# Kernel tuning notes

Hardware: AMD Instinct MI355X
Metric: run time of the kernel (lower is better)

The kernel has to match this reference:

```python
import jax, jax.numpy as jnp
import numpy as np

ALPHA = 0.2  # LeakyReLU negative slope


def setup_inputs() -> dict:
    key = jax.random.key(0)
    k1, k2, k3, k4 = jax.random.split(key, 4)
    bs, n, fin = 8, 1024, 256
    heads, fo = 8, 64
    h = jax.random.normal(k1, (bs, n, fin), dtype=jnp.float32)
    adj = jax.random.randint(k2, (bs, n, n), 0, 2, dtype=jnp.int32)
    # W stored as [in_features, heads*out] so Wh = h @ W (same math as torch Linear)
    W = jax.random.normal(k3, (fin, heads * fo), dtype=jnp.float32) * 0.1
    a = jax.random.normal(k4, (heads, 2 * fo), dtype=jnp.float32) * 0.1
    return {"h": h, "adj": adj, "W": W, "a": a}


def reference(h, adj, W, a):
    bs, n, _ = h.shape
    heads, two_fo = a.shape
    fo = two_fo // 2
    # Wh: [bs, n, heads, fo]
    Wh = (h @ W).reshape(bs, n, heads, fo)
    a_src, a_dst = a[:, :fo], a[:, fo:]
    # Additive attention decomposed: e[b,h,i,j] = leaky_relu(src[b,h,i] + dst[b,h,j])
    e_src = jnp.einsum('bnhf,hf->bhn', Wh, a_src)  # [bs, heads, n]
    e_dst = jnp.einsum('bnhf,hf->bhn', Wh, a_dst)
    e = e_src[:, :, :, None] + e_dst[:, :, None, :]  # [bs, heads, n, n]
    e = jnp.where(e > 0, e, ALPHA * e)  # LeakyReLU
    e = jnp.where(adj[:, None, :, :] == 0, -jnp.inf, e)
    attn = jax.nn.softmax(e, axis=-1)  # [bs, heads, n, n]
    # h_prime[b,i,h,f] = sum_j attn[b,h,i,j] * Wh[b,j,h,f]
    h_prime = jnp.einsum('bhij,bjhf->bihf', attn, Wh)
    return h_prime.reshape(bs, n, heads * fo)
```

## Files before the change

kernel.cpp:

```cpp
#include <hip/hip_runtime.h>
#include <hip/hip_bf16.h>
#include <math.h>

#define BS 8
#define NN 1024
#define FIN 256
#define HEADS 8
#define FO 64
#define NH (HEADS*FO)
static constexpr float ALPHA = 0.2f;
static constexpr float LOG2E = 1.4426950408889634f;

typedef short bf16x8 __attribute__((ext_vector_type(8)));
typedef float f32x4  __attribute__((ext_vector_type(4)));
typedef unsigned short u16;
typedef unsigned u32;
typedef u16 u16x4v __attribute__((ext_vector_type(4)));
typedef u16 u16x8v __attribute__((ext_vector_type(8)));

__device__ __forceinline__ u16 f2b(float x) {
    __hip_bfloat16 b = __float2bfloat16(x);
    return *reinterpret_cast<u16*>(&b);
}
__device__ __forceinline__ float fexp2(float x) {
#if __has_builtin(__builtin_amdgcn_exp2f)
    return __builtin_amdgcn_exp2f(x);
#else
    float r; asm("v_exp_f32 %0, %1" : "=v"(r) : "v"(x)); return r;
#endif
}
__device__ __forceinline__ void gload_lds16(const void* g, void* l) {
    __builtin_amdgcn_global_load_lds(
        (const __attribute__((address_space(1))) unsigned int*)g,
        (__attribute__((address_space(3))) unsigned int*)l, 16, 0, 0);
}

__global__ __launch_bounds__(256) void prep_misc(const float* __restrict__ h,
                                                 const int* __restrict__ adj,
                                                 const float* __restrict__ W,
                                                 u16* __restrict__ hb,
                                                 u16* __restrict__ WbT,
                                                 u32* __restrict__ bits) {
    const int bid = blockIdx.x;
    const int t = threadIdx.x;
    if (bid < 8192) {
        const int lane = t & 63;
        const size_t e0 = ((size_t)bid * 256 + t) * 4;
        const int4 v = *reinterpret_cast<const int4*>(adj + e0);
        u32 x = (v.x ? 1u : 0u) | (v.y ? 2u : 0u) | (v.z ? 4u : 0u) | (v.w ? 8u : 0u);
        {   const u32 r = (u32)__shfl_xor((int)x, 1);
            const int sh = (lane & 1) * 4;  x = (x << sh) | (r << (4 - sh)); }
        {   const u32 r = (u32)__shfl_xor((int)x, 2);
            const int sh = (lane & 2) * 4;  x = (x << sh) | (r << (8 - sh)); }
        {   const u32 r = (u32)__shfl_xor((int)x, 4);
            const int sh = (lane & 4) * 4;  x = (x << sh) | (r << (16 - sh)); }
        if ((lane & 7) == 0) bits[e0 >> 5] = x;
    } else if (bid < 9216) {
        const int i = ((bid - 8192) * 256 + t) * 8;
        const float4 v0 = *reinterpret_cast<const float4*>(h + i);
        const float4 v1 = *reinterpret_cast<const float4*>(h + i + 4);
        u16x8v o;
        o[0]=f2b(v0.x); o[1]=f2b(v0.y); o[2]=f2b(v0.z); o[3]=f2b(v0.w);
        o[4]=f2b(v1.x); o[5]=f2b(v1.y); o[6]=f2b(v1.z); o[7]=f2b(v1.w);
        *reinterpret_cast<u16x8v*>(hb + i) = o;
    } else {
        __shared__ float T[64][65];
        const int bb = bid - 9216;
        const int hh = bb & 7;
        const int n0 = hh * 64, k0 = (bb >> 3) * 64;
        const int r4 = t >> 6, c = t & 63;
        #pragma unroll
        for (int p = 0; p < 16; ++p) {
            const int r = p * 4 + r4;
            T[r][c] = W[(size_t)(k0 + r) * NH + n0 + c];
        }
        __syncthreads();
        #pragma unroll
        for (int p = 0; p < 16; ++p) {
            const int r = p * 4 + r4;
            WbT[(size_t)(n0 + r) * FIN + k0 + c] = f2b(T[c][r]);
        }
    }
}

__global__ __launch_bounds__(256) void gemm_whT(const u16* __restrict__ hb,
                                                const u16* __restrict__ WbT,
                                                const float* __restrict__ avec,
                                                u16* __restrict__ WhT,
                                                float* __restrict__ esrc,
                                                float* __restrict__ edst) {
    __shared__ u16 Al[2][64 * 64];
    __shared__ u16 Bl[2][64 * 64];
    const int t = threadIdx.x, wv = t >> 6, lane = t & 63;
    const int g = lane >> 4, l15 = lane & 15;
    const int lid = (blockIdx.x & 7) * 128 + (blockIdx.x >> 3);
    const int m0 = (lid >> 3) * 64;
    const int h  = lid & 7;
    const int lr = lane >> 3;
    const int sch = (lane & 7) ^ lr;
    const int bh = (m0 >> 10) * HEADS + h;

    f32x4 acc[4] = {};

    auto stageA = [&](int buf, int k0) {
        #pragma unroll
        for (int c = 0; c < 2; ++c) {
            const int rowb = wv * 16 + c * 8;
            gload_lds16(hb + (size_t)(m0 + rowb + lr) * FIN + k0 + sch * 8,
                        &Al[buf][rowb * 64]);
        }
    };
    auto stageB = [&](int buf, int k0) {
        #pragma unroll
        for (int c = 0; c < 2; ++c) {
            const int rowb = wv * 16 + c * 8;
            gload_lds16(WbT + (size_t)(h * 64 + rowb + lr) * FIN + k0 + sch * 8,
                        &Bl[buf][rowb * 64]);
        }
    };

    stageA(0, 0); stageB(0, 0);
    __syncthreads();
    for (int kt = 0; kt < 4; ++kt) {
        const int buf = kt & 1;
        if (kt < 3) { stageA(buf ^ 1, (kt + 1) * 64); stageB(buf ^ 1, (kt + 1) * 64); }
        #pragma unroll
        for (int ks = 0; ks < 2; ++ks) {
            const int ch = (ks * 4 + g) ^ (l15 & 7);
            const bf16x8 afr = *reinterpret_cast<const bf16x8*>(
                &Al[buf][(wv * 16 + l15) * 64 + ch * 8]);
            #pragma unroll
            for (int n = 0; n < 4; ++n) {
                const bf16x8 bfr = *reinterpret_cast<const bf16x8*>(
                    &Bl[buf][(n * 16 + l15) * 64 + ch * 8]);
                acc[n] = __builtin_amdgcn_mfma_f32_16x16x32_bf16(afr, bfr, acc[n], 0, 0, 0);
            }
        }
        __syncthreads();
    }

    {
        float as_[4], ad_[4];
        #pragma unroll
        for (int n = 0; n < 4; ++n) {
            as_[n] = avec[h * 128 + n * 16 + l15] * LOG2E;
            ad_[n] = avec[h * 128 + 64 + n * 16 + l15] * LOG2E;
        }
        #pragma unroll
        for (int r = 0; r < 4; ++r) {
            float ps = acc[0][r] * as_[0] + acc[1][r] * as_[1]
                     + acc[2][r] * as_[2] + acc[3][r] * as_[3];
            float pd = acc[0][r] * ad_[0] + acc[1][r] * ad_[1]
                     + acc[2][r] * ad_[2] + acc[3][r] * ad_[3];
            #pragma unroll
            for (int off = 1; off < 16; off <<= 1) {
                ps += __shfl_xor(ps, off);
                pd += __shfl_xor(pd, off);
            }
            if (l15 == 0) {
                const int i = (m0 + wv * 16 + g * 4 + r) & (NN - 1);
                esrc[(size_t)bh * NN + i] = ps;
                edst[(size_t)bh * NN + i] = pd;
            }
        }
    }

    u16* scr = &Al[0][0];
    #pragma unroll
    for (int n = 0; n < 4; ++n) {
        u16x4v pk;
        #pragma unroll
        for (int r = 0; r < 4; ++r) pk[r] = f2b(acc[n][r]);
        *reinterpret_cast<u16x4v*>(&scr[(n * 16 + l15) * 72 + wv * 16 + g * 4]) = pk;
    }
    __syncthreads();
    const int il0 = m0 & (NN - 1);
    const int f = t >> 2, q = t & 3;
    const u16x8v v0 = *reinterpret_cast<const u16x8v*>(&scr[f * 72 + q * 16]);
    const u16x8v v1 = *reinterpret_cast<const u16x8v*>(&scr[f * 72 + q * 16 + 8]);
    u16* dst = &WhT[((size_t)bh * 64 + f) * NN + il0 + q * 16];
    *reinterpret_cast<u16x8v*>(dst)     = v0;
    *reinterpret_cast<u16x8v*>(dst + 8) = v1;
}

__global__ __launch_bounds__(128, 4) void attn_pv(const u32* __restrict__ bits,
                                                  const u16* __restrict__ WhT,
                                                  const float* __restrict__ esrc,
                                                  const float* __restrict__ edst,
                                                  float* __restrict__ out) {
    __shared__ u16 Bs[2][64 * 64];
    const int t = threadIdx.x, wv = t >> 6, lane = t & 63;
    const int g = lane >> 4, l15 = lane & 15;
    const int lr = lane >> 3, sch = (lane & 7) ^ lr;

    const int lid = (blockIdx.x & 7) * 256 + (blockIdx.x >> 3);
    const int it = lid & 31, h = (lid >> 5) & 7, b = lid >> 8;
    const int i0 = it * 32;
    const int bh = b * HEADS + h;
    const int rowi = i0 + wv * 16 + l15;

    const float es = esrc[(size_t)bh * NN + rowi];
    const u16*  whb = WhT + (size_t)bh * 64 * NN;
    const float* ed = edst + (size_t)bh * NN + 8 * g;
    const u32*  bitrow = bits + (size_t)(b * NN + rowi) * 32;

    auto stageB = [&](int buf, int j0) {
        #pragma unroll
        for (int c = 0; c < 4; ++c) {
            const int fb = wv * 32 + c * 8;
            gload_lds16(whb + (size_t)(fb + lr) * NN + j0 + sch * 8,
                        &Bs[buf][fb * 64]);
        }
    };

    stageB(0, 0);
    float4 peA[2], peB[2];
    u32    pwS[2];
    #pragma unroll
    for (int s = 0; s < 2; ++s) {
        peA[s] = *(const float4*)(ed + s * 32);
        peB[s] = *(const float4*)(ed + s * 32 + 4);
        pwS[s] = bitrow[s];
    }
    __syncthreads();

    f32x4 acc[4] = {};
    f32x4 dsum = {};
    bf16x8 ones;
    #pragma unroll
    for (int q = 0; q < 8; ++q) ones[q] = (short)0x3F80;

    for (int tt = 0; tt < 16; ++tt) {
        const int buf = tt & 1;
        const bool more = (tt < 15);
        if (more) {
            stageB(buf ^ 1, (tt + 1) * 64);
            asm volatile("" ::: "memory");
        }
        #pragma unroll
        for (int ks = 0; ks < 2; ++ks) {
            const int s = tt * 2 + ks;
            const float4 e0 = peA[ks], e1 = peB[ks];
            const u32 word = pwS[ks];
            if (more) {
                peA[ks] = *(const float4*)(ed + (s + 2) * 32);
                peB[ks] = *(const float4*)(ed + (s + 2) * 32 + 4);
                pwS[ks] = bitrow[s + 2];
            }
            const int chb = ((ks * 4 + g) ^ (l15 & 7)) * 8;
            const bf16x8 v0 = *(const bf16x8*)(&Bs[buf][(0 * 16 + l15) * 64 + chb]);
            const bf16x8 v1 = *(const bf16x8*)(&Bs[buf][(1 * 16 + l15) * 64 + chb]);
            const bf16x8 v2 = *(const bf16x8*)(&Bs[buf][(2 * 16 + l15) * 64 + chb]);
            const bf16x8 v3 = *(const bf16x8*)(&Bs[buf][(3 * 16 + l15) * 64 + chb]);

            const u32 byte_ = (word >> (8 * g)) & 0xffu;
            float ps[8];
            {
                float sv;
                sv = es + e0.x; sv = fmaxf(sv, ALPHA * sv); sv = (byte_ & 1u)        ? sv : -1e30f; ps[0] = fexp2(sv);
                sv = es + e0.y; sv = fmaxf(sv, ALPHA * sv); sv = ((byte_ >> 1) & 1u) ? sv : -1e30f; ps[1] = fexp2(sv);
                sv = es + e0.z; sv = fmaxf(sv, ALPHA * sv); sv = ((byte_ >> 2) & 1u) ? sv : -1e30f; ps[2] = fexp2(sv);
                sv = es + e0.w; sv = fmaxf(sv, ALPHA * sv); sv = ((byte_ >> 3) & 1u) ? sv : -1e30f; ps[3] = fexp2(sv);
                sv = es + e1.x; sv = fmaxf(sv, ALPHA * sv); sv = ((byte_ >> 4) & 1u) ? sv : -1e30f; ps[4] = fexp2(sv);
                sv = es + e1.y; sv = fmaxf(sv, ALPHA * sv); sv = ((byte_ >> 5) & 1u) ? sv : -1e30f; ps[5] = fexp2(sv);
                sv = es + e1.z; sv = fmaxf(sv, ALPHA * sv); sv = ((byte_ >> 6) & 1u) ? sv : -1e30f; ps[6] = fexp2(sv);
                sv = es + e1.w; sv = fmaxf(sv, ALPHA * sv); sv = ((byte_ >> 7) & 1u) ? sv : -1e30f; ps[7] = fexp2(sv);
            }
            union { u32 u[4]; bf16x8 v; } af;
            #pragma unroll
            for (int qp = 0; qp < 4; ++qp) {
                union { __hip_bfloat162 b2; u32 w; } cv;
                cv.b2 = __float22bfloat162_rn(make_float2(ps[2*qp], ps[2*qp+1]));
                af.u[qp] = cv.w;
            }
            __builtin_amdgcn_s_setprio(1);
            acc[0] = __builtin_amdgcn_mfma_f32_16x16x32_bf16(af.v, v0, acc[0], 0, 0, 0);
            acc[1] = __builtin_amdgcn_mfma_f32_16x16x32_bf16(af.v, v1, acc[1], 0, 0, 0);
            acc[2] = __builtin_amdgcn_mfma_f32_16x16x32_bf16(af.v, v2, acc[2], 0, 0, 0);
            acc[3] = __builtin_amdgcn_mfma_f32_16x16x32_bf16(af.v, v3, acc[3], 0, 0, 0);
            dsum   = __builtin_amdgcn_mfma_f32_16x16x32_bf16(af.v, ones, dsum, 0, 0, 0);
            __builtin_amdgcn_s_setprio(0);
        }
        if (more) {
            asm volatile("s_waitcnt vmcnt(6)" ::: "memory");
            __builtin_amdgcn_s_barrier();
        }
    }

    float inv[4];
    #pragma unroll
    for (int r = 0; r < 4; ++r) inv[r] = 1.0f / dsum[r];
    #pragma unroll
    for (int n = 0; n < 4; ++n)
        #pragma unroll
        for (int r = 0; r < 4; ++r) {
            const int io = i0 + wv * 16 + g * 4 + r;
            out[(size_t)(b * NN + io) * NH + h * 64 + n * 16 + l15] =
                acc[n][r] * inv[r];
        }
}

extern "C" void kernel_launch(void* const* d_in, const int* in_sizes, int n_in,
                              void* d_out, int out_size, void* d_ws, size_t ws_size,
                              hipStream_t stream) {
    const float* h   = (const float*)d_in[0];
    const int*   adj = (const int*)  d_in[1];
    const float* W   = (const float*)d_in[2];
    const float* a   = (const float*)d_in[3];
    float* out = (float*)d_out;

    char* p = (char*)d_ws;
    u16*   hb   = (u16*)p;   p += (size_t)BS * NN * FIN * 2;
    u16*   WbT  = (u16*)p;   p += (size_t)NH * FIN * 2;
    u16*   WhT  = (u16*)p;   p += (size_t)BS * HEADS * FO * NN * 2;
    float* esrc = (float*)p; p += (size_t)BS * HEADS * NN * 4;
    float* edst = (float*)p; p += (size_t)BS * HEADS * NN * 4;
    u32*   bits = (u32*)p;

    prep_misc<<<9248, 256, 0, stream>>>(h, adj, W, hb, WbT, bits);
    gemm_whT <<<1024, 256, 0, stream>>>(hb, WbT, a, WhT, esrc, edst);
    attn_pv  <<<2048, 128, 0, stream>>>(bits, WhT, esrc, edst, out);
}
```

Before: 51.35 us.

## Enlarge attention tile to 128 rows per block with two row-groups per wave

The attention-PV kernel now runs 4 waves per block, each handling 32 query rows instead of 16, so a block covers 128 rows. Each staged WhT tile in shared memory and each LDS B-fragment read is reused across two MFMA row groups. This cuts the global and LDS traffic per output row and the number of blocks. In exchange the kernel uses more registers per wave (two accumulator sets), has fewer blocks (512) to spread across CUs, and its wait count was adjusted to match the new load count.

```diff
diff --git a/kernel.cpp b/kernel.cpp
--- a/kernel.cpp
+++ b/kernel.cpp
@@ -183,7 +183,7 @@
     *reinterpret_cast<u16x8v*>(dst + 8) = v1;
 }
 
-__global__ __launch_bounds__(128, 4) void attn_pv(const u32* __restrict__ bits,
+__global__ __launch_bounds__(256, 2) void attn_pv(const u32* __restrict__ bits,
                                                   const u16* __restrict__ WhT,
                                                   const float* __restrict__ esrc,
                                                   const float* __restrict__ edst,
@@ -193,21 +193,23 @@
     const int g = lane >> 4, l15 = lane & 15;
     const int lr = lane >> 3, sch = (lane & 7) ^ lr;
 
-    const int lid = (blockIdx.x & 7) * 256 + (blockIdx.x >> 3);
-    const int it = lid & 31, h = (lid >> 5) & 7, b = lid >> 8;
-    const int i0 = it * 32;
+    const int lid = (blockIdx.x & 7) * 64 + (blockIdx.x >> 3);
+    const int it = lid & 7, h = (lid >> 3) & 7, b = lid >> 6;
+    const int i0 = it * 128;
     const int bh = b * HEADS + h;
-    const int rowi = i0 + wv * 16 + l15;
-
-    const float es = esrc[(size_t)bh * NN + rowi];
+    const int row0 = i0 + wv * 32 + l15;
+
+    const float es0 = esrc[(size_t)bh * NN + row0];
+    const float es1 = esrc[(size_t)bh * NN + row0 + 16];
     const u16*  whb = WhT + (size_t)bh * 64 * NN;
     const float* ed = edst + (size_t)bh * NN + 8 * g;
-    const u32*  bitrow = bits + (size_t)(b * NN + rowi) * 32;
+    const u32*  bitrow0 = bits + (size_t)(b * NN + row0) * 32;
+    const u32*  bitrow1 = bitrow0 + 16 * 32;
 
     auto stageB = [&](int buf, int j0) {
         #pragma unroll
-        for (int c = 0; c < 4; ++c) {
-            const int fb = wv * 32 + c * 8;
+        for (int c = 0; c < 2; ++c) {
+            const int fb = wv * 16 + c * 8;
             gload_lds16(whb + (size_t)(fb + lr) * NN + j0 + sch * 8,
                         &Bs[buf][fb * 64]);
         }
@@ -215,17 +217,18 @@
 
     stageB(0, 0);
     float4 peA[2], peB[2];
-    u32    pwS[2];
+    u32    pw0[2], pw1[2];
     #pragma unroll
     for (int s = 0; s < 2; ++s) {
         peA[s] = *(const float4*)(ed + s * 32);
         peB[s] = *(const float4*)(ed + s * 32 + 4);
-        pwS[s] = bitrow[s];
+        pw0[s] = bitrow0[s];
+        pw1[s] = bitrow1[s];
     }
     __syncthreads();
 
-    f32x4 acc[4] = {};
-    f32x4 dsum = {};
+    f32x4 acc0[4] = {}, acc1[4] = {};
+    f32x4 dsum0 = {}, dsum1 = {};
     bf16x8 ones;
     #pragma unroll
     for (int q = 0; q < 8; ++q) ones[q] = (short)0x3F80;
@@ -241,11 +244,12 @@
         for (int ks = 0; ks < 2; ++ks) {
             const int s = tt * 2 + ks;
             const float4 e0 = peA[ks], e1 = peB[ks];
-            const u32 word = pwS[ks];
+            const u32 w0 = pw0[ks], w1 = pw1[ks];
             if (more) {
                 peA[ks] = *(const float4*)(ed + (s + 2) * 32);
                 peB[ks] = *(const float4*)(ed + (s + 2) * 32 + 4);
-                pwS[ks] = bitrow[s + 2];
+                pw0[ks] = bitrow0[s + 2];
+                pw1[ks] = bitrow1[s + 2];
             }
             const int chb = ((ks * 4 + g) ^ (l15 & 7)) * 8;
             const bf16x8 v0 = *(const bf16x8*)(&Bs[buf][(0 * 16 + l15) * 64 + chb]);
@@ -253,50 +257,63 @@
             const bf16x8 v2 = *(const bf16x8*)(&Bs[buf][(2 * 16 + l15) * 64 + chb]);
             const bf16x8 v3 = *(const bf16x8*)(&Bs[buf][(3 * 16 + l15) * 64 + chb]);
 
-            const u32 byte_ = (word >> (8 * g)) & 0xffu;
-            float ps[8];
-            {
-                float sv;
-                sv = es + e0.x; sv = fmaxf(sv, ALPHA * sv); sv = (byte_ & 1u)        ? sv : -1e30f; ps[0] = fexp2(sv);
-                sv = es + e0.y; sv = fmaxf(sv, ALPHA * sv); sv = ((byte_ >> 1) & 1u) ? sv : -1e30f; ps[1] = fexp2(sv);
-                sv = es + e0.z; sv = fmaxf(sv, ALPHA * sv); sv = ((byte_ >> 2) & 1u) ? sv : -1e30f; ps[2] = fexp2(sv);
-                sv = es + e0.w; sv = fmaxf(sv, ALPHA * sv); sv = ((byte_ >> 3) & 1u) ? sv : -1e30f; ps[3] = fexp2(sv);
-                sv = es + e1.x; sv = fmaxf(sv, ALPHA * sv); sv = ((byte_ >> 4) & 1u) ? sv : -1e30f; ps[4] = fexp2(sv);
-                sv = es + e1.y; sv = fmaxf(sv, ALPHA * sv); sv = ((byte_ >> 5) & 1u) ? sv : -1e30f; ps[5] = fexp2(sv);
-                sv = es + e1.z; sv = fmaxf(sv, ALPHA * sv); sv = ((byte_ >> 6) & 1u) ? sv : -1e30f; ps[6] = fexp2(sv);
-                sv = es + e1.w; sv = fmaxf(sv, ALPHA * sv); sv = ((byte_ >> 7) & 1u) ? sv : -1e30f; ps[7] = fexp2(sv);
-            }
-            union { u32 u[4]; bf16x8 v; } af;
+            float ej[8];
+            ej[0]=e0.x; ej[1]=e0.y; ej[2]=e0.z; ej[3]=e0.w;
+            ej[4]=e1.x; ej[5]=e1.y; ej[6]=e1.z; ej[7]=e1.w;
+            const u32 by0 = (w0 >> (8 * g)) & 0xffu;
+            const u32 by1 = (w1 >> (8 * g)) & 0xffu;
+            float p0[8], p1[8];
+            #pragma unroll
+            for (int q = 0; q < 8; ++q) {
+                float s0 = es0 + ej[q];
+                float s1 = es1 + ej[q];
+                s0 = fmaxf(s0, ALPHA * s0);
+                s1 = fmaxf(s1, ALPHA * s1);
+                s0 = ((by0 >> q) & 1u) ? s0 : -1e30f;
+                s1 = ((by1 >> q) & 1u) ? s1 : -1e30f;
+                p0[q] = fexp2(s0);
+                p1[q] = fexp2(s1);
+            }
+            union { u32 u[4]; bf16x8 v; } af0, af1;
             #pragma unroll
             for (int qp = 0; qp < 4; ++qp) {
-                union { __hip_bfloat162 b2; u32 w; } cv;
-                cv.b2 = __float22bfloat162_rn(make_float2(ps[2*qp], ps[2*qp+1]));
-                af.u[qp] = cv.w;
+                union { __hip_bfloat162 b2; u32 w; } c0, c1;
+                c0.b2 = __float22bfloat162_rn(make_float2(p0[2*qp], p0[2*qp+1]));
+                c1.b2 = __float22bfloat162_rn(make_float2(p1[2*qp], p1[2*qp+1]));
+                af0.u[qp] = c0.w;
+                af1.u[qp] = c1.w;
             }
             __builtin_amdgcn_s_setprio(1);
-            acc[0] = __builtin_amdgcn_mfma_f32_16x16x32_bf16(af.v, v0, acc[0], 0, 0, 0);
-            acc[1] = __builtin_amdgcn_mfma_f32_16x16x32_bf16(af.v, v1, acc[1], 0, 0, 0);
-            acc[2] = __builtin_amdgcn_mfma_f32_16x16x32_bf16(af.v, v2, acc[2], 0, 0, 0);
-            acc[3] = __builtin_amdgcn_mfma_f32_16x16x32_bf16(af.v, v3, acc[3], 0, 0, 0);
-            dsum   = __builtin_amdgcn_mfma_f32_16x16x32_bf16(af.v, ones, dsum, 0, 0, 0);
+            acc0[0] = __builtin_amdgcn_mfma_f32_16x16x32_bf16(af0.v, v0, acc0[0], 0, 0, 0);
+            acc1[0] = __builtin_amdgcn_mfma_f32_16x16x32_bf16(af1.v, v0, acc1[0], 0, 0, 0);
+            acc0[1] = __builtin_amdgcn_mfma_f32_16x16x32_bf16(af0.v, v1, acc0[1], 0, 0, 0);
+            acc1[1] = __builtin_amdgcn_mfma_f32_16x16x32_bf16(af1.v, v1, acc1[1], 0, 0, 0);
+            acc0[2] = __builtin_amdgcn_mfma_f32_16x16x32_bf16(af0.v, v2, acc0[2], 0, 0, 0);
+            acc1[2] = __builtin_amdgcn_mfma_f32_16x16x32_bf16(af1.v, v2, acc1[2], 0, 0, 0);
+            acc0[3] = __builtin_amdgcn_mfma_f32_16x16x32_bf16(af0.v, v3, acc0[3], 0, 0, 0);
+            acc1[3] = __builtin_amdgcn_mfma_f32_16x16x32_bf16(af1.v, v3, acc1[3], 0, 0, 0);
+            dsum0   = __builtin_amdgcn_mfma_f32_16x16x32_bf16(af0.v, ones, dsum0, 0, 0, 0);
+            dsum1   = __builtin_amdgcn_mfma_f32_16x16x32_bf16(af1.v, ones, dsum1, 0, 0, 0);
             __builtin_amdgcn_s_setprio(0);
         }
         if (more) {
-            asm volatile("s_waitcnt vmcnt(6)" ::: "memory");
+            asm volatile("s_waitcnt vmcnt(8)" ::: "memory");
             __builtin_amdgcn_s_barrier();
         }
     }
 
-    float inv[4];
-    #pragma unroll
-    for (int r = 0; r < 4; ++r) inv[r] = 1.0f / dsum[r];
+    float inv0[4], inv1[4];
+    #pragma unroll
+    for (int r = 0; r < 4; ++r) { inv0[r] = 1.0f / dsum0[r]; inv1[r] = 1.0f / dsum1[r]; }
     #pragma unroll
     for (int n = 0; n < 4; ++n)
         #pragma unroll
         for (int r = 0; r < 4; ++r) {
-            const int io = i0 + wv * 16 + g * 4 + r;
-            out[(size_t)(b * NN + io) * NH + h * 64 + n * 16 + l15] =
-                acc[n][r] * inv[r];
+            const int io0 = i0 + wv * 32 + g * 4 + r;
+            out[(size_t)(b * NN + io0) * NH + h * 64 + n * 16 + l15] =
+                acc0[n][r] * inv0[r];
+            out[(size_t)(b * NN + io0 + 16) * NH + h * 64 + n * 16 + l15] =
+                acc1[n][r] * inv1[r];
         }
 }
 
@@ -319,5 +336,5 @@
 
     prep_misc<<<9248, 256, 0, stream>>>(h, adj, W, hb, WbT, bits);
     gemm_whT <<<1024, 256, 0, stream>>>(hb, WbT, a, WhT, esrc, edst);
-    attn_pv  <<<2048, 128, 0, stream>>>(bits, WhT, esrc, edst, out);
-}
+    attn_pv  <<<512, 256, 0, stream>>>(bits, WhT, esrc, edst, out);
+}
```

Result: faster. 50.30 us (-2.0%).

## Remap attn_pv so each wave owns a head with private V buffers, no barriers

Applied to the files above, without the earlier changes.

The attention-PV kernel now gives each 256-thread block 16 query rows and 4 heads, with one wave per head. Each wave streams its own V tiles into a private double-buffered LDS region, so the per-iteration block barrier is dropped. The adjacency bit words for the 16 rows are loaded into shared memory once and shared across the four head-waves, rather than fetched per wave from global memory. The trade-offs are a smaller 16-row tile per wave, 32 narrower pipeline steps, and reliance on the vmcnt wait alone to keep the intra-wave LDS double buffering correct.

```diff
diff --git a/kernel.cpp b/kernel.cpp
--- a/kernel.cpp
+++ b/kernel.cpp
@@ -183,46 +183,57 @@
     *reinterpret_cast<u16x8v*>(dst + 8) = v1;
 }
 
-__global__ __launch_bounds__(128, 4) void attn_pv(const u32* __restrict__ bits,
+__global__ __launch_bounds__(256, 4) void attn_pv(const u32* __restrict__ bits,
                                                   const u16* __restrict__ WhT,
                                                   const float* __restrict__ esrc,
                                                   const float* __restrict__ edst,
                                                   float* __restrict__ out) {
-    __shared__ u16 Bs[2][64 * 64];
+    __shared__ u16 Vb[4][2][2048];
+    __shared__ u32 bitsT[32][16];
+
     const int t = threadIdx.x, wv = t >> 6, lane = t & 63;
     const int g = lane >> 4, l15 = lane & 15;
-    const int lr = lane >> 3, sch = (lane & 7) ^ lr;
-
-    const int lid = (blockIdx.x & 7) * 256 + (blockIdx.x >> 3);
-    const int it = lid & 31, h = (lid >> 5) & 7, b = lid >> 8;
-    const int i0 = it * 32;
+
+    const int lid = (blockIdx.x & 7) * 128 + (blockIdx.x >> 3);
+    const int it = lid & 63;
+    const int combo = lid >> 6;
+    const int b = combo >> 1, hg = combo & 1;
+    const int i0 = it * 16;
+    const int h  = hg * 4 + wv;
     const int bh = b * HEADS + h;
-    const int rowi = i0 + wv * 16 + l15;
-
-    const float es = esrc[(size_t)bh * NN + rowi];
+
+    const float es = esrc[(size_t)bh * NN + i0 + l15];
     const u16*  whb = WhT + (size_t)bh * 64 * NN;
     const float* ed = edst + (size_t)bh * NN + 8 * g;
-    const u32*  bitrow = bits + (size_t)(b * NN + rowi) * 32;
-
-    auto stageB = [&](int buf, int j0) {
+
+    auto stage = [&](int buf, int j0) {
+        const int fr  = lane >> 2;
+        const int jc  = (lane & 3) ^ ((lane >> 3) & 3);
         #pragma unroll
         for (int c = 0; c < 4; ++c) {
-            const int fb = wv * 32 + c * 8;
-            gload_lds16(whb + (size_t)(fb + lr) * NN + j0 + sch * 8,
-                        &Bs[buf][fb * 64]);
+            gload_lds16(whb + (size_t)(c * 16 + fr) * NN + j0 + jc * 8,
+                        &Vb[wv][buf][c * 512]);
         }
     };
 
-    stageB(0, 0);
+    {
+        const int r = t & 15, w2 = t >> 4;
+        const u32* src = bits + (size_t)(b * NN + i0 + r) * 32 + w2 * 2;
+        bitsT[w2 * 2 + 0][r] = src[0];
+        bitsT[w2 * 2 + 1][r] = src[1];
+    }
+    stage(0, 0);
     float4 peA[2], peB[2];
-    u32    pwS[2];
     #pragma unroll
     for (int s = 0; s < 2; ++s) {
         peA[s] = *(const float4*)(ed + s * 32);
         peB[s] = *(const float4*)(ed + s * 32 + 4);
-        pwS[s] = bitrow[s];
     }
     __syncthreads();
+    u32 pw = bitsT[0][l15];
+
+    const int bsB = l15 * 64 + ((g ^ ((l15 >> 1) & 3)) << 4);
+    const char* vwave = (const char*)&Vb[wv][0][0];
 
     f32x4 acc[4] = {};
     f32x4 dsum = {};
@@ -230,61 +241,52 @@
     #pragma unroll
     for (int q = 0; q < 8; ++q) ones[q] = (short)0x3F80;
 
-    for (int tt = 0; tt < 16; ++tt) {
+    for (int tt = 0; tt < 32; ++tt) {
         const int buf = tt & 1;
-        const bool more = (tt < 15);
-        if (more) {
-            stageB(buf ^ 1, (tt + 1) * 64);
-            asm volatile("" ::: "memory");
-        }
-        #pragma unroll
-        for (int ks = 0; ks < 2; ++ks) {
-            const int s = tt * 2 + ks;
-            const float4 e0 = peA[ks], e1 = peB[ks];
-            const u32 word = pwS[ks];
-            if (more) {
-                peA[ks] = *(const float4*)(ed + (s + 2) * 32);
-                peB[ks] = *(const float4*)(ed + (s + 2) * 32 + 4);
-                pwS[ks] = bitrow[s + 2];
-            }
-            const int chb = ((ks * 4 + g) ^ (l15 & 7)) * 8;
-            const bf16x8 v0 = *(const bf16x8*)(&Bs[buf][(0 * 16 + l15) * 64 + chb]);
-            const bf16x8 v1 = *(const bf16x8*)(&Bs[buf][(1 * 16 + l15) * 64 + chb]);
-            const bf16x8 v2 = *(const bf16x8*)(&Bs[buf][(2 * 16 + l15) * 64 + chb]);
-            const bf16x8 v3 = *(const bf16x8*)(&Bs[buf][(3 * 16 + l15) * 64 + chb]);
-
-            const u32 byte_ = (word >> (8 * g)) & 0xffu;
-            float ps[8];
-            {
-                float sv;
-                sv = es + e0.x; sv = fmaxf(sv, ALPHA * sv); sv = (byte_ & 1u)        ? sv : -1e30f; ps[0] = fexp2(sv);
-                sv = es + e0.y; sv = fmaxf(sv, ALPHA * sv); sv = ((byte_ >> 1) & 1u) ? sv : -1e30f; ps[1] = fexp2(sv);
-                sv = es + e0.z; sv = fmaxf(sv, ALPHA * sv); sv = ((byte_ >> 2) & 1u) ? sv : -1e30f; ps[2] = fexp2(sv);
-                sv = es + e0.w; sv = fmaxf(sv, ALPHA * sv); sv = ((byte_ >> 3) & 1u) ? sv : -1e30f; ps[3] = fexp2(sv);
-                sv = es + e1.x; sv = fmaxf(sv, ALPHA * sv); sv = ((byte_ >> 4) & 1u) ? sv : -1e30f; ps[4] = fexp2(sv);
-                sv = es + e1.y; sv = fmaxf(sv, ALPHA * sv); sv = ((byte_ >> 5) & 1u) ? sv : -1e30f; ps[5] = fexp2(sv);
-                sv = es + e1.z; sv = fmaxf(sv, ALPHA * sv); sv = ((byte_ >> 6) & 1u) ? sv : -1e30f; ps[6] = fexp2(sv);
-                sv = es + e1.w; sv = fmaxf(sv, ALPHA * sv); sv = ((byte_ >> 7) & 1u) ? sv : -1e30f; ps[7] = fexp2(sv);
-            }
-            union { u32 u[4]; bf16x8 v; } af;
-            #pragma unroll
-            for (int qp = 0; qp < 4; ++qp) {
-                union { __hip_bfloat162 b2; u32 w; } cv;
-                cv.b2 = __float22bfloat162_rn(make_float2(ps[2*qp], ps[2*qp+1]));
-                af.u[qp] = cv.w;
-            }
-            __builtin_amdgcn_s_setprio(1);
-            acc[0] = __builtin_amdgcn_mfma_f32_16x16x32_bf16(af.v, v0, acc[0], 0, 0, 0);
-            acc[1] = __builtin_amdgcn_mfma_f32_16x16x32_bf16(af.v, v1, acc[1], 0, 0, 0);
-            acc[2] = __builtin_amdgcn_mfma_f32_16x16x32_bf16(af.v, v2, acc[2], 0, 0, 0);
-            acc[3] = __builtin_amdgcn_mfma_f32_16x16x32_bf16(af.v, v3, acc[3], 0, 0, 0);
-            dsum   = __builtin_amdgcn_mfma_f32_16x16x32_bf16(af.v, ones, dsum, 0, 0, 0);
-            __builtin_amdgcn_s_setprio(0);
-        }
-        if (more) {
-            asm volatile("s_waitcnt vmcnt(6)" ::: "memory");
-            __builtin_amdgcn_s_barrier();
-        }
+        const int jn = (tt < 31) ? (tt + 1) * 32 : 31 * 32;
+        const int en = (tt < 30) ? (tt + 2) * 32 : 31 * 32;
+        stage(buf ^ 1, jn);
+        asm volatile("" ::: "memory");
+        const float4 e0 = peA[buf], e1 = peB[buf];
+        const u32 word = pw;
+        peA[buf] = *(const float4*)(ed + en);
+        peB[buf] = *(const float4*)(ed + en + 4);
+        pw = bitsT[(tt < 31) ? tt + 1 : 31][l15];
+        asm volatile("s_waitcnt vmcnt(6)" ::: "memory");
+
+        const char* vb = vwave + buf * 4096 + bsB;
+        const bf16x8 v0 = *(const bf16x8*)(vb);
+        const bf16x8 v1 = *(const bf16x8*)(vb + 1024);
+        const bf16x8 v2 = *(const bf16x8*)(vb + 2048);
+        const bf16x8 v3 = *(const bf16x8*)(vb + 3072);
+
+        const u32 byte_ = (word >> (8 * g)) & 0xffu;
+        float ps[8];
+        {
+            float sv;
+            sv = es + e0.x; sv = fmaxf(sv, ALPHA * sv); sv = (byte_ & 1u)        ? sv : -1e30f; ps[0] = fexp2(sv);
+            sv = es + e0.y; sv = fmaxf(sv, ALPHA * sv); sv = ((byte_ >> 1) & 1u) ? sv : -1e30f; ps[1] = fexp2(sv);
+            sv = es + e0.z; sv = fmaxf(sv, ALPHA * sv); sv = ((byte_ >> 2) & 1u) ? sv : -1e30f; ps[2] = fexp2(sv);
+            sv = es + e0.w; sv = fmaxf(sv, ALPHA * sv); sv = ((byte_ >> 3) & 1u) ? sv : -1e30f; ps[3] = fexp2(sv);
+            sv = es + e1.x; sv = fmaxf(sv, ALPHA * sv); sv = ((byte_ >> 4) & 1u) ? sv : -1e30f; ps[4] = fexp2(sv);
+            sv = es + e1.y; sv = fmaxf(sv, ALPHA * sv); sv = ((byte_ >> 5) & 1u) ? sv : -1e30f; ps[5] = fexp2(sv);
+            sv = es + e1.z; sv = fmaxf(sv, ALPHA * sv); sv = ((byte_ >> 6) & 1u) ? sv : -1e30f; ps[6] = fexp2(sv);
+            sv = es + e1.w; sv = fmaxf(sv, ALPHA * sv); sv = ((byte_ >> 7) & 1u) ? sv : -1e30f; ps[7] = fexp2(sv);
+        }
+        union { u32 u[4]; bf16x8 v; } af;
+        #pragma unroll
+        for (int qp = 0; qp < 4; ++qp) {
+            union { __hip_bfloat162 b2; u32 w; } cv;
+            cv.b2 = __float22bfloat162_rn(make_float2(ps[2*qp], ps[2*qp+1]));
+            af.u[qp] = cv.w;
+        }
+        __builtin_amdgcn_s_setprio(1);
+        acc[0] = __builtin_amdgcn_mfma_f32_16x16x32_bf16(af.v, v0, acc[0], 0, 0, 0);
+        acc[1] = __builtin_amdgcn_mfma_f32_16x16x32_bf16(af.v, v1, acc[1], 0, 0, 0);
+        acc[2] = __builtin_amdgcn_mfma_f32_16x16x32_bf16(af.v, v2, acc[2], 0, 0, 0);
+        acc[3] = __builtin_amdgcn_mfma_f32_16x16x32_bf16(af.v, v3, acc[3], 0, 0, 0);
+        dsum   = __builtin_amdgcn_mfma_f32_16x16x32_bf16(af.v, ones, dsum, 0, 0, 0);
+        __builtin_amdgcn_s_setprio(0);
     }
 
     float inv[4];
@@ -294,7 +296,7 @@
     for (int n = 0; n < 4; ++n)
         #pragma unroll
         for (int r = 0; r < 4; ++r) {
-            const int io = i0 + wv * 16 + g * 4 + r;
+            const int io = i0 + g * 4 + r;
             out[(size_t)(b * NN + io) * NH + h * 64 + n * 16 + l15] =
                 acc[n][r] * inv[r];
         }
@@ -319,5 +321,5 @@
 
     prep_misc<<<9248, 256, 0, stream>>>(h, adj, W, hb, WbT, bits);
     gemm_whT <<<1024, 256, 0, stream>>>(hb, WbT, a, WhT, esrc, edst);
-    attn_pv  <<<2048, 128, 0, stream>>>(bits, WhT, esrc, edst, out);
-}
+    attn_pv  <<<1024, 256, 0, stream>>>(bits, WhT, esrc, edst, out);
+}
```

Result: slower. 110.7 us (+115.7%).

## Enlarge projection GEMM tiles to 128x128 and triple-buffer attention PV loads

Applied to the files above, without the earlier changes.

The Wh projection GEMM now computes 128x128 tiles with a 2x2 wave layout and 4x4 MFMA fragments per wave, covering two heads per block. This cuts the grid from 1024 to 256 blocks and improves operand reuse from shared memory, at the cost of more registers and fewer blocks in flight. The attention PV kernel moves from a two-stage to a three-stage shared-memory ring with prefetch distance 2 and looser vmcnt waits, with occupancy bound lowered to 3 blocks per SM, to hide global load latency.

```diff
diff --git a/kernel.cpp b/kernel.cpp
--- a/kernel.cpp
+++ b/kernel.cpp
@@ -89,32 +89,37 @@
                                                 u16* __restrict__ WhT,
                                                 float* __restrict__ esrc,
                                                 float* __restrict__ edst) {
-    __shared__ u16 Al[2][64 * 64];
-    __shared__ u16 Bl[2][64 * 64];
+    __shared__ u16 Al[2][128 * 64];
+    __shared__ u16 Bl[2][128 * 64];
     const int t = threadIdx.x, wv = t >> 6, lane = t & 63;
     const int g = lane >> 4, l15 = lane & 15;
-    const int lid = (blockIdx.x & 7) * 128 + (blockIdx.x >> 3);
-    const int m0 = (lid >> 3) * 64;
-    const int h  = lid & 7;
     const int lr = lane >> 3;
     const int sch = (lane & 7) ^ lr;
-    const int bh = (m0 >> 10) * HEADS + h;
-
-    f32x4 acc[4] = {};
+
+    const int lid = (blockIdx.x & 7) * 32 + (blockIdx.x >> 3);
+    const int mt = lid >> 2, nt = lid & 3;
+    const int m0 = mt * 128;
+    const int b  = mt >> 3;
+    const int il0 = (mt & 7) * 128;
+    const int wm = wv >> 1, wn = wv & 1;
+    const int head = nt * 2 + wn;
+    const int bh = b * HEADS + head;
+
+    f32x4 acc[4][4] = {};
 
     auto stageA = [&](int buf, int k0) {
         #pragma unroll
-        for (int c = 0; c < 2; ++c) {
-            const int rowb = wv * 16 + c * 8;
+        for (int c = 0; c < 4; ++c) {
+            const int rowb = wv * 32 + c * 8;
             gload_lds16(hb + (size_t)(m0 + rowb + lr) * FIN + k0 + sch * 8,
                         &Al[buf][rowb * 64]);
         }
     };
     auto stageB = [&](int buf, int k0) {
         #pragma unroll
-        for (int c = 0; c < 2; ++c) {
-            const int rowb = wv * 16 + c * 8;
-            gload_lds16(WbT + (size_t)(h * 64 + rowb + lr) * FIN + k0 + sch * 8,
+        for (int c = 0; c < 4; ++c) {
+            const int rowb = wv * 32 + c * 8;
+            gload_lds16(WbT + (size_t)(nt * 128 + rowb + lr) * FIN + k0 + sch * 8,
                         &Bl[buf][rowb * 64]);
         }
     };
@@ -127,14 +132,21 @@
         #pragma unroll
         for (int ks = 0; ks < 2; ++ks) {
             const int ch = (ks * 4 + g) ^ (l15 & 7);
-            const bf16x8 afr = *reinterpret_cast<const bf16x8*>(
-                &Al[buf][(wv * 16 + l15) * 64 + ch * 8]);
-            #pragma unroll
-            for (int n = 0; n < 4; ++n) {
-                const bf16x8 bfr = *reinterpret_cast<const bf16x8*>(
-                    &Bl[buf][(n * 16 + l15) * 64 + ch * 8]);
-                acc[n] = __builtin_amdgcn_mfma_f32_16x16x32_bf16(afr, bfr, acc[n], 0, 0, 0);
-            }
+            bf16x8 af[4], bf[4];
+            #pragma unroll
+            for (int mf = 0; mf < 4; ++mf)
+                af[mf] = *reinterpret_cast<const bf16x8*>(
+                    &Al[buf][(wm * 64 + mf * 16 + l15) * 64 + ch * 8]);
+            #pragma unroll
+            for (int n = 0; n < 4; ++n)
+                bf[n] = *reinterpret_cast<const bf16x8*>(
+                    &Bl[buf][(wn * 64 + n * 16 + l15) * 64 + ch * 8]);
+            #pragma unroll
+            for (int mf = 0; mf < 4; ++mf)
+                #pragma unroll
+                for (int n = 0; n < 4; ++n)
+                    acc[mf][n] = __builtin_amdgcn_mfma_f32_16x16x32_bf16(
+                        af[mf], bf[n], acc[mf][n], 0, 0, 0);
         }
         __syncthreads();
     }
@@ -143,52 +155,62 @@
         float as_[4], ad_[4];
         #pragma unroll
         for (int n = 0; n < 4; ++n) {
-            as_[n] = avec[h * 128 + n * 16 + l15] * LOG2E;
-            ad_[n] = avec[h * 128 + 64 + n * 16 + l15] * LOG2E;
-        }
-        #pragma unroll
-        for (int r = 0; r < 4; ++r) {
-            float ps = acc[0][r] * as_[0] + acc[1][r] * as_[1]
-                     + acc[2][r] * as_[2] + acc[3][r] * as_[3];
-            float pd = acc[0][r] * ad_[0] + acc[1][r] * ad_[1]
-                     + acc[2][r] * ad_[2] + acc[3][r] * ad_[3];
-            #pragma unroll
-            for (int off = 1; off < 16; off <<= 1) {
-                ps += __shfl_xor(ps, off);
-                pd += __shfl_xor(pd, off);
+            as_[n] = avec[head * 128 + n * 16 + l15] * LOG2E;
+            ad_[n] = avec[head * 128 + 64 + n * 16 + l15] * LOG2E;
+        }
+        #pragma unroll
+        for (int mf = 0; mf < 4; ++mf)
+            #pragma unroll
+            for (int r = 0; r < 4; ++r) {
+                float ps = acc[mf][0][r] * as_[0] + acc[mf][1][r] * as_[1]
+                         + acc[mf][2][r] * as_[2] + acc[mf][3][r] * as_[3];
+                float pd = acc[mf][0][r] * ad_[0] + acc[mf][1][r] * ad_[1]
+                         + acc[mf][2][r] * ad_[2] + acc[mf][3][r] * ad_[3];
+                #pragma unroll
+                for (int off = 1; off < 16; off <<= 1) {
+                    ps += __shfl_xor(ps, off);
+                    pd += __shfl_xor(pd, off);
+                }
+                if (l15 == 0) {
+                    const int i = il0 + wm * 64 + mf * 16 + g * 4 + r;
+                    esrc[(size_t)bh * NN + i] = ps;
+                    edst[(size_t)bh * NN + i] = pd;
+                }
             }
-            if (l15 == 0) {
-                const int i = (m0 + wv * 16 + g * 4 + r) & (NN - 1);
-                esrc[(size_t)bh * NN + i] = ps;
-                edst[(size_t)bh * NN + i] = pd;
-            }
-        }
-    }
-
-    u16* scr = &Al[0][0];
-    #pragma unroll
-    for (int n = 0; n < 4; ++n) {
-        u16x4v pk;
-        #pragma unroll
-        for (int r = 0; r < 4; ++r) pk[r] = f2b(acc[n][r]);
-        *reinterpret_cast<u16x4v*>(&scr[(n * 16 + l15) * 72 + wv * 16 + g * 4]) = pk;
-    }
+    }
+
+    u16* scrH = wn ? &Bl[0][0] : &Al[0][0];
+    #pragma unroll
+    for (int mf = 0; mf < 4; ++mf)
+        #pragma unroll
+        for (int n = 0; n < 4; ++n) {
+            u16x4v pk;
+            #pragma unroll
+            for (int r = 0; r < 4; ++r) pk[r] = f2b(acc[mf][n][r]);
+            *reinterpret_cast<u16x4v*>(
+                &scrH[(n * 16 + l15) * 132 + wm * 64 + mf * 16 + g * 4]) = pk;
+        }
     __syncthreads();
-    const int il0 = m0 & (NN - 1);
-    const int f = t >> 2, q = t & 3;
-    const u16x8v v0 = *reinterpret_cast<const u16x8v*>(&scr[f * 72 + q * 16]);
-    const u16x8v v1 = *reinterpret_cast<const u16x8v*>(&scr[f * 72 + q * 16 + 8]);
-    u16* dst = &WhT[((size_t)bh * 64 + f) * NN + il0 + q * 16];
-    *reinterpret_cast<u16x8v*>(dst)     = v0;
-    *reinterpret_cast<u16x8v*>(dst + 8) = v1;
-}
-
-__global__ __launch_bounds__(128, 4) void attn_pv(const u32* __restrict__ bits,
+    {
+        const int hsel = t >> 7;
+        const int f    = (t >> 1) & 63;
+        const int seg  = t & 1;
+        const u16* src = (hsel ? &Bl[0][0] : &Al[0][0]) + f * 132 + seg * 64;
+        u16* dst = &WhT[((size_t)(b * HEADS + nt * 2 + hsel) * 64 + f) * NN
+                        + il0 + seg * 64];
+        #pragma unroll
+        for (int k = 0; k < 8; ++k)
+            *reinterpret_cast<u16x8v*>(dst + k * 8) =
+                *reinterpret_cast<const u16x8v*>(src + k * 8);
+    }
+}
+
+__global__ __launch_bounds__(128, 3) void attn_pv(const u32* __restrict__ bits,
                                                   const u16* __restrict__ WhT,
                                                   const float* __restrict__ esrc,
                                                   const float* __restrict__ edst,
                                                   float* __restrict__ out) {
-    __shared__ u16 Bs[2][64 * 64];
+    __shared__ u16 Bs[3][64 * 64];
     const int t = threadIdx.x, wv = t >> 6, lane = t & 63;
     const int g = lane >> 4, l15 = lane & 15;
     const int lr = lane >> 3, sch = (lane & 7) ^ lr;
@@ -204,7 +226,7 @@
     const float* ed = edst + (size_t)bh * NN + 8 * g;
     const u32*  bitrow = bits + (size_t)(b * NN + rowi) * 32;
 
-    auto stageB = [&](int buf, int j0) {
+    auto stage = [&](int buf, int j0) {
         #pragma unroll
         for (int c = 0; c < 4; ++c) {
             const int fb = wv * 32 + c * 8;
@@ -213,7 +235,8 @@
         }
     };
 
-    stageB(0, 0);
+    stage(0, 0);
+    stage(1, 64);
     float4 peA[2], peB[2];
     u32    pwS[2];
     #pragma unroll
@@ -222,7 +245,8 @@
         peB[s] = *(const float4*)(ed + s * 32 + 4);
         pwS[s] = bitrow[s];
     }
-    __syncthreads();
+    asm volatile("s_waitcnt vmcnt(10)" ::: "memory");
+    __builtin_amdgcn_s_barrier();
 
     f32x4 acc[4] = {};
     f32x4 dsum = {};
@@ -230,28 +254,29 @@
     #pragma unroll
     for (int q = 0; q < 8; ++q) ones[q] = (short)0x3F80;
 
+    int bufR = 0, bufW = 2;
     for (int tt = 0; tt < 16; ++tt) {
-        const int buf = tt & 1;
-        const bool more = (tt < 15);
-        if (more) {
-            stageB(buf ^ 1, (tt + 1) * 64);
-            asm volatile("" ::: "memory");
-        }
+        const int jn = (tt < 14) ? (tt + 2) * 64 : 15 * 64;
+        stage(bufW, jn);
+        asm volatile("" ::: "memory");
+        const int bsBase = bufR * 8192;
         #pragma unroll
         for (int ks = 0; ks < 2; ++ks) {
             const int s = tt * 2 + ks;
             const float4 e0 = peA[ks], e1 = peB[ks];
             const u32 word = pwS[ks];
-            if (more) {
-                peA[ks] = *(const float4*)(ed + (s + 2) * 32);
-                peB[ks] = *(const float4*)(ed + (s + 2) * 32 + 4);
-                pwS[ks] = bitrow[s + 2];
+            {
+                const int sn = (s < 30) ? s + 2 : 31;
+                peA[ks] = *(const float4*)(ed + sn * 32);
+                peB[ks] = *(const float4*)(ed + sn * 32 + 4);
+                pwS[ks] = bitrow[sn];
             }
-            const int chb = ((ks * 4 + g) ^ (l15 & 7)) * 8;
-            const bf16x8 v0 = *(const bf16x8*)(&Bs[buf][(0 * 16 + l15) * 64 + chb]);
-            const bf16x8 v1 = *(const bf16x8*)(&Bs[buf][(1 * 16 + l15) * 64 + chb]);
-            const bf16x8 v2 = *(const bf16x8*)(&Bs[buf][(2 * 16 + l15) * 64 + chb]);
-            const bf16x8 v3 = *(const bf16x8*)(&Bs[buf][(3 * 16 + l15) * 64 + chb]);
+            const char* bsb = (const char*)Bs + bsBase
+                            + l15 * 128 + (((ks * 4 + g) ^ (l15 & 7)) << 4);
+            const bf16x8 v0 = *(const bf16x8*)(bsb);
+            const bf16x8 v1 = *(const bf16x8*)(bsb + 2048);
+            const bf16x8 v2 = *(const bf16x8*)(bsb + 4096);
+            const bf16x8 v3 = *(const bf16x8*)(bsb + 6144);
 
             const u32 byte_ = (word >> (8 * g)) & 0xffu;
             float ps[8];
@@ -281,10 +306,12 @@
             dsum   = __builtin_amdgcn_mfma_f32_16x16x32_bf16(af.v, ones, dsum, 0, 0, 0);
             __builtin_amdgcn_s_setprio(0);
         }
-        if (more) {
-            asm volatile("s_waitcnt vmcnt(6)" ::: "memory");
+        if (tt < 15) {
+            asm volatile("s_waitcnt vmcnt(16)" ::: "memory");
             __builtin_amdgcn_s_barrier();
         }
+        bufR = (bufR == 2) ? 0 : bufR + 1;
+        bufW = (bufW == 2) ? 0 : bufW + 1;
     }
 
     float inv[4];
@@ -318,6 +345,6 @@
     u32*   bits = (u32*)p;
 
     prep_misc<<<9248, 256, 0, stream>>>(h, adj, W, hb, WbT, bits);
-    gemm_whT <<<1024, 256, 0, stream>>>(hb, WbT, a, WhT, esrc, edst);
+    gemm_whT <<<256, 256, 0, stream>>>(hb, WbT, a, WhT, esrc, edst);
     attn_pv  <<<2048, 128, 0, stream>>>(bits, WhT, esrc, edst, out);
 }
```

After: 65.32 us. 27.2% more time.
